# Kernel optimization log

Hardware: AMD Instinct MI355X
Metric: run time of the kernel (lower is better)

The kernel has to match this reference:

```python
import jax, jax.numpy as jnp
import numpy as np

B, IN, E, NCLS = 1024, 784, 256, 10
BRAIN, ADIM, NJUMPS = 4, 3, 4
N = BRAIN ** ADIM  # 64 blocks
TAU = 1.0
_GKEY = jax.random.key(42)  # fixed key -> deterministic gumbel noise


def _gumbel_softmax_hard(key, logits):
    u = jax.random.uniform(key, logits.shape, minval=1e-6, maxval=1.0 - 1e-6)
    g = -jnp.log(-jnp.log(u))
    y = jax.nn.softmax((logits + g) / TAU, axis=-1)
    hard = jax.nn.one_hot(jnp.argmax(y, axis=-1), logits.shape[-1], dtype=y.dtype)
    return jax.lax.stop_gradient(hard - y) + y  # straight-through


def _next_address(state, key, at0_W1, at0_b1, at0_W2, at0_b2):
    # always uses block 0's address_transform (as in the original forward)
    h = jax.nn.relu(state @ at0_W1 + at0_b1)
    logits = (h @ at0_W2 + at0_b2).reshape(state.shape[0], ADIM, BRAIN)
    return _gumbel_softmax_hard(key, logits)  # (B, ADIM, BRAIN) one-hot


def _all_blocks(state, st_W1, st_b1, st_W2, st_b2):
    # state: (B,E); st_W*: (N,E,E) stored (in,out). Two batched GEMMs over all N blocks.
    h = jax.nn.relu(jnp.einsum('be,neh->bnh', state, st_W1) + st_b1[None])
    h = jax.nn.relu(jnp.einsum('bnh,nhg->bng', h, st_W2) + st_b2[None])
    norm = jnp.linalg.norm(state, axis=1, keepdims=True)  # (B,1), norm of INPUT state
    return h / (norm[:, :, None] + 1e-6)  # (B,N,E)


def _flatten_onehot(oh):
    # (B, ADIM, BRAIN) -> (B, BRAIN**ADIM) via iterated outer product
    b = oh.shape[0]
    fw = oh[:, 0, :]
    for d in range(1, oh.shape[1]):
        fw = (fw[:, :, None] * oh[:, d, None, :]).reshape(b, -1)
    return fw


def _forward(x, W_emb, b_emb, st_W1, st_b1, st_W2, st_b2,
             at0_W1, at0_b1, at0_W2, at0_b2, out_W1, out_b1, out_W2, out_b2):
    bsz = x.shape[0]
    state = x.reshape(bsz, -1) @ W_emb + b_emb
    initial_state = state
    current_address = _next_address(state, jax.random.fold_in(_GKEY, 0),
                                    at0_W1, at0_b1, at0_W2, at0_b2)
    exited = jnp.zeros((bsz,), dtype=bool)
    exit_states = jnp.zeros_like(state)
    exit_addresses = jnp.zeros_like(current_address)
    for i in range(NJUMPS):  # fixed small jump count; early-break replaced by masking (same math)
        active = ~exited
        bw = _flatten_onehot(current_address)                      # (B,N)
        allout = _all_blocks(state, st_W1, st_b1, st_W2, st_b2)    # (B,N,E)
        new_state = jnp.einsum('bn,bne->be', bw, allout)
        new_address = _next_address(new_state, jax.random.fold_in(_GKEY, i + 1),
                                    at0_W1, at0_b1, at0_W2, at0_b2)
        idx = jnp.argmax(new_address, axis=2)
        is_origin = jnp.all(idx == 0, axis=1) & active
        exit_states = jnp.where(is_origin[:, None], new_state, exit_states)
        exit_addresses = jnp.where(is_origin[:, None, None], new_address, exit_addresses)
        exited = exited | is_origin
        state = jnp.where(active[:, None], new_state, state)
        current_address = jnp.where(active[:, None, None], new_address, current_address)
    final_address = jnp.where(exited[:, None, None], exit_addresses, current_address)
    bw = _flatten_onehot(final_address)
    # original code computes block_out twice and keeps the one using `state` (bug-faithful)
    allout = _all_blocks(state, st_W1, st_b1, st_W2, st_b2)
    final_output = jnp.einsum('bn,bne->be', bw, allout) + initial_state
    h = jax.nn.relu(final_output @ out_W1 + out_b1)
    return h @ out_W2 + out_b2  # (B, NCLS)


def setup_inputs() -> dict:
    key = jax.random.key(0)
    ks = jax.random.split(key, 16)
    s = 0.02
    return {
        'x': jax.random.normal(ks[0], (B, IN), jnp.float32),
        'W_emb': jax.random.normal(ks[1], (IN, E), jnp.float32) * s,
        'b_emb': jnp.zeros((E,), jnp.float32),
        'st_W1': jax.random.normal(ks[2], (N, E, E), jnp.float32) * s,
        'st_b1': jnp.zeros((N, E), jnp.float32),
        'st_W2': jax.random.normal(ks[3], (N, E, E), jnp.float32) * s,
        'st_b2': jnp.zeros((N, E), jnp.float32),
        'at0_W1': jax.random.normal(ks[4], (E, E), jnp.float32) * s,
        'at0_b1': jnp.zeros((E,), jnp.float32),
        'at0_W2': jax.random.normal(ks[5], (E, ADIM * BRAIN), jnp.float32) * s,
        'at0_b2': jnp.zeros((ADIM * BRAIN,), jnp.float32),
        'out_W1': jax.random.normal(ks[6], (E, E), jnp.float32) * s,
        'out_b1': jnp.zeros((E,), jnp.float32),
        'out_W2': jax.random.normal(ks[7], (E, NCLS), jnp.float32) * s,
        'out_b2': jnp.zeros((NCLS,), jnp.float32),
    }


def reference(x, W_emb, b_emb, st_W1, st_b1, st_W2, st_b2,
              at0_W1, at0_b1, at0_W2, at0_b2, out_W1, out_b1, out_W2, out_b2):
    return _forward(x, W_emb, b_emb, st_W1, st_b1, st_W2, st_b2,
                    at0_W1, at0_b1, at0_W2, at0_b2, out_W1, out_b1, out_W2, out_b2)
```

## Files before the change

kernel.cpp:

```cpp
#include <hip/hip_runtime.h>
#include <stdint.h>


#define BATCH 1024
#define EDIM  256
#define INDIM 784
#define CH    4
#define GRID_B 304

__host__ __device__ inline uint32_t rotl32(uint32_t x, uint32_t d) {
  return (x << d) | (x >> (32u - d));
}
__host__ __device__ inline void threefry2x32(uint32_t k0, uint32_t k1,
                                             uint32_t x0, uint32_t x1,
                                             uint32_t* o0, uint32_t* o1) {
  uint32_t ks2 = k0 ^ k1 ^ 0x1BD11BDAu;
  x0 += k0; x1 += k1;
#define TF_R(a) { x0 += x1; x1 = rotl32(x1, a); x1 ^= x0; }
  TF_R(13) TF_R(15) TF_R(26) TF_R(6)   x0 += k1;  x1 += ks2 + 1u;
  TF_R(17) TF_R(29) TF_R(16) TF_R(24)  x0 += ks2; x1 += k0  + 2u;
  TF_R(13) TF_R(15) TF_R(26) TF_R(6)   x0 += k0;  x1 += k1  + 3u;
  TF_R(17) TF_R(29) TF_R(16) TF_R(24)  x0 += k1;  x1 += ks2 + 4u;
  TF_R(13) TF_R(15) TF_R(26) TF_R(6)   x0 += ks2; x1 += k0  + 5u;
#undef TF_R
  *o0 = x0; *o1 = x1;
}
__device__ inline uint32_t jax_bits12288(uint32_t k0, uint32_t k1, uint32_t L) {
  uint32_t o0, o1;
  if (L < 6144u) { threefry2x32(k0, k1, L, L + 6144u, &o0, &o1); return o0; }
  else           { threefry2x32(k0, k1, L - 6144u, L, &o0, &o1); return o1; }
}
__device__ inline float jax_uniform(uint32_t bits) {
  const float minv = 1e-6f;
  const float maxv = (float)(1.0 - 1e-06);
  const float span = maxv - minv;
  uint32_t fb = (bits >> 9) | 0x3f800000u;
  float f = __uint_as_float(fb) - 1.0f;
  float u = __fadd_rn(__fmul_rn(f, span), minv);
  return fmaxf(minv, u);
}
__device__ inline float gumbel_val(int s, int b, int c) {
  uint32_t fk0, fk1;
  threefry2x32(0u, 42u, 0u, (uint32_t)s, &fk0, &fk1);
  const uint32_t L = (uint32_t)(b * 12 + c);
  const float u = jax_uniform(jax_bits12288(fk0, fk1, L));
  return -logf(-logf(u));
}
__device__ inline int addr_argmax(const float* v) {
  int i0 = 0, i1 = 0, i2 = 0;
  { float b = v[0];
    for (int c = 1; c < 4; c++) { float x = v[c];     if (x > b) { b = x; i0 = c; } } }
  { float b = v[4];
    for (int c = 1; c < 4; c++) { float x = v[4 + c]; if (x > b) { b = x; i1 = c; } } }
  { float b = v[8];
    for (int c = 1; c < 4; c++) { float x = v[8 + c]; if (x > b) { b = x; i2 = c; } } }
  return i0 * 16 + i1 * 4 + i2;
}

#define LDW16(dst, Wc, kkq)                                                     \
  { _Pragma("unroll")                                                           \
    for (int _q = 0; _q < 4; _q++) {                                            \
      _Pragma("unroll")                                                         \
      for (int _cc = 0; _cc < 4; _cc++)                                         \
        dst[_q * 4 + _cc] = (Wc)[(size_t)((kkq) + _q) * EDIM + _cc * 64];       \
    } }

#define FMA16(acc, wv, XSarr, SROW, kabs)                                       \
  { const float4 _r0 = *(const float4*)&(XSarr)[0 * (SROW) + (kabs)];           \
    const float4 _r1 = *(const float4*)&(XSarr)[1 * (SROW) + (kabs)];           \
    const float4 _r2 = *(const float4*)&(XSarr)[2 * (SROW) + (kabs)];           \
    const float4 _r3 = *(const float4*)&(XSarr)[3 * (SROW) + (kabs)];           \
    _Pragma("unroll")                                                           \
    for (int _cc = 0; _cc < 4; _cc++) {                                         \
      acc[0][_cc] = fmaf(_r0.x, wv[0 + _cc], acc[0][_cc]);                      \
      acc[0][_cc] = fmaf(_r0.y, wv[4 + _cc], acc[0][_cc]);                      \
      acc[0][_cc] = fmaf(_r0.z, wv[8 + _cc], acc[0][_cc]);                      \
      acc[0][_cc] = fmaf(_r0.w, wv[12 + _cc], acc[0][_cc]);                     \
      acc[1][_cc] = fmaf(_r1.x, wv[0 + _cc], acc[1][_cc]);                      \
      acc[1][_cc] = fmaf(_r1.y, wv[4 + _cc], acc[1][_cc]);                      \
      acc[1][_cc] = fmaf(_r1.z, wv[8 + _cc], acc[1][_cc]);                      \
      acc[1][_cc] = fmaf(_r1.w, wv[12 + _cc], acc[1][_cc]);                     \
      acc[2][_cc] = fmaf(_r2.x, wv[0 + _cc], acc[2][_cc]);                      \
      acc[2][_cc] = fmaf(_r2.y, wv[4 + _cc], acc[2][_cc]);                      \
      acc[2][_cc] = fmaf(_r2.z, wv[8 + _cc], acc[2][_cc]);                      \
      acc[2][_cc] = fmaf(_r2.w, wv[12 + _cc], acc[2][_cc]);                     \
      acc[3][_cc] = fmaf(_r3.x, wv[0 + _cc], acc[3][_cc]);                      \
      acc[3][_cc] = fmaf(_r3.y, wv[4 + _cc], acc[3][_cc]);                      \
      acc[3][_cc] = fmaf(_r3.z, wv[8 + _cc], acc[3][_cc]);                      \
      acc[3][_cc] = fmaf(_r3.w, wv[12 + _cc], acc[3][_cc]);                     \
    } }

#define GEMM_TILE(Wbase, XSarr, SROW, kb, KS, acc)                              \
  { const float* _Wc = (Wbase) + (size_t)(kb) * EDIM + jc;                      \
    float _wvA[16], _wvB[16];                                                   \
    LDW16(_wvA, _Wc, 0)                                                         \
    _Pragma("unroll 1")                                                         \
    for (int _kk = 0; _kk < (KS); _kk += 8) {                                   \
      LDW16(_wvB, _Wc, _kk + 4)                                                 \
      FMA16(acc, _wvA, XSarr, SROW, (kb) + _kk)                                 \
      if (_kk + 8 < (KS)) LDW16(_wvA, _Wc, _kk + 8)                             \
      FMA16(acc, _wvB, XSarr, SROW, (kb) + _kk + 4)                             \
    } }

#define FMA16H(acc, wv, Harr, kabs)                                             \
  { _Pragma("unroll")                                                           \
    for (int _q = 0; _q < 4; _q++) {                                            \
      const float4 _h = *(const float4*)&(Harr)[((kabs) + _q) * 4];             \
      _Pragma("unroll")                                                         \
      for (int _cc = 0; _cc < 4; _cc++) {                                       \
        acc[0][_cc] = fmaf(_h.x, wv[_q * 4 + _cc], acc[0][_cc]);                \
        acc[1][_cc] = fmaf(_h.y, wv[_q * 4 + _cc], acc[1][_cc]);                \
        acc[2][_cc] = fmaf(_h.z, wv[_q * 4 + _cc], acc[2][_cc]);                \
        acc[3][_cc] = fmaf(_h.w, wv[_q * 4 + _cc], acc[3][_cc]);                \
      } } }

#define GEMM_TILE_H(Wbase, Harr, kb, KS, acc)                                   \
  { const float* _Wc = (Wbase) + (size_t)(kb) * EDIM + jc;                      \
    float _wvA[16], _wvB[16];                                                   \
    LDW16(_wvA, _Wc, 0)                                                         \
    _Pragma("unroll 1")                                                         \
    for (int _kk = 0; _kk < (KS); _kk += 8) {                                   \
      LDW16(_wvB, _Wc, _kk + 4)                                                 \
      FMA16H(acc, _wvA, Harr, (kb) + _kk)                                       \
      if (_kk + 8 < (KS)) LDW16(_wvA, _Wc, _kk + 8)                             \
      FMA16H(acc, _wvB, Harr, (kb) + _kk + 4)                                   \
    } }

#define P_STORE(P, kg, jc, acc)                                                 \
  { _Pragma("unroll")                                                           \
    for (int _cc = 0; _cc < 4; _cc++) {                                         \
      const int _col = (jc) + _cc * 64;                                         \
      *(float4*)&(P)[(((kg) * 256) + _col) * 4] =                               \
        make_float4(acc[0][_cc], acc[1][_cc], acc[2][_cc], acc[3][_cc]);        \
    } }

#define P_REDUCE8(P, col, bias, dst4)                                           \
  { float4 _ps = *(const float4*)&(P)[(col) * 4];                               \
    _Pragma("unroll")                                                           \
    for (int _pw = 1; _pw < 8; _pw++) {                                         \
      const float4 _pp = *(const float4*)&(P)[((_pw * 256) + (col)) * 4];       \
      _ps.x += _pp.x; _ps.y += _pp.y; _ps.z += _pp.z; _ps.w += _pp.w;           \
    }                                                                           \
    _ps.x += (bias); _ps.y += (bias); _ps.z += (bias); _ps.w += (bias);         \
    dst4 = _ps; }

#define ADDR_TAIL(P, H, P2a, vals, ab1, aW2, ab2, astep, b0)                    \
  { if (t < 256) {                                                              \
      float4 s; P_REDUCE8(P, t, (ab1)[t], s);                                   \
      *(float4*)&(H)[t * 4] = make_float4(fmaxf(s.x, 0.f), fmaxf(s.y, 0.f),     \
                                          fmaxf(s.z, 0.f), fmaxf(s.w, 0.f));    \
    }                                                                           \
    __syncthreads();                                                            \
    { const int c = t & 15, ksl = t >> 4;                                       \
      float a2[4] = {0.f, 0.f, 0.f, 0.f};                                       \
      if (c < 12) {                                                             \
        const int k0 = ksl * 8;                                                 \
        _Pragma("unroll")                                                       \
        for (int k = k0; k < k0 + 8; k++) {                                     \
          const float4 h = *(const float4*)&(H)[k * 4];                         \
          const float w = (aW2)[k * 12 + c];                                    \
          a2[0] = fmaf(h.x, w, a2[0]); a2[1] = fmaf(h.y, w, a2[1]);             \
          a2[2] = fmaf(h.z, w, a2[2]); a2[3] = fmaf(h.w, w, a2[3]);             \
        }                                                                       \
      }                                                                         \
      *(float4*)&(P2a)[(ksl * 16 + c) * 4] = make_float4(a2[0], a2[1], a2[2], a2[3]); \
    }                                                                           \
    __syncthreads();                                                            \
    if (t < 48) {                                                               \
      const int i = t / 12, c = t % 12;                                         \
      float s = 0.f;                                                            \
      _Pragma("unroll")                                                         \
      for (int w = 0; w < 32; w++) s += (P2a)[(w * 16 + c) * 4 + i];            \
      (vals)[i * 12 + c] = s + (ab2)[c] + gumbel_val((astep), (b0) + i, c);     \
    }                                                                           \
    __syncthreads();                                                            \
  }

__global__ __launch_bounds__(512, 2) void k_embed_a0(
    const float* __restrict__ x, const float* __restrict__ Wemb,
    const float* __restrict__ bemb,
    const float* __restrict__ aW1, const float* __restrict__ ab1,
    const float* __restrict__ aW2, const float* __restrict__ ab2,
    float* __restrict__ state, float* __restrict__ initial,
    int* __restrict__ nn_all) {
  __shared__ __align__(16) float XS[4 * INDIM];
  __shared__ __align__(16) float P[8 * 256 * 4];
  __shared__ __align__(16) float SS[4 * EDIM];
  __shared__ __align__(16) float H[EDIM * 4];
  __shared__ __align__(16) float P2a[32 * 16 * 4];
  __shared__ float vals[4 * 12];
  const int t = threadIdx.x, b0 = blockIdx.x * 4;
  const int jc = t & 63, kg = t >> 6;

  { const float4* src = (const float4*)(x + (size_t)b0 * INDIM);
    for (int p = t; p < INDIM; p += 512) ((float4*)XS)[p] = src[p];
  }
  __syncthreads();

  {
    const int kb = (kg < 2) ? kg * 104 : 208 + (kg - 2) * 96;
    float acc[4][4] = {};
    if (kg < 2) { GEMM_TILE(Wemb, XS, INDIM, kb, 104, acc); }
    else        { GEMM_TILE(Wemb, XS, INDIM, kb, 96, acc); }
    P_STORE(P, kg, jc, acc);
  }
  __syncthreads();
  if (t < 256) {
    float4 s; P_REDUCE8(P, t, bemb[t], s);
    SS[0 * EDIM + t] = s.x; SS[1 * EDIM + t] = s.y;
    SS[2 * EDIM + t] = s.z; SS[3 * EDIM + t] = s.w;
    state[(size_t)(b0 + 0) * EDIM + t] = s.x; initial[(size_t)(b0 + 0) * EDIM + t] = s.x;
    state[(size_t)(b0 + 1) * EDIM + t] = s.y; initial[(size_t)(b0 + 1) * EDIM + t] = s.y;
    state[(size_t)(b0 + 2) * EDIM + t] = s.z; initial[(size_t)(b0 + 2) * EDIM + t] = s.z;
    state[(size_t)(b0 + 3) * EDIM + t] = s.w; initial[(size_t)(b0 + 3) * EDIM + t] = s.w;
  }
  __syncthreads();

  {
    const int kb = kg * 32;
    float acc[4][4] = {};
    GEMM_TILE(aW1, SS, EDIM, kb, 32, acc);
    P_STORE(P, kg, jc, acc);
  }
  __syncthreads();
  ADDR_TAIL(P, H, P2a, vals, ab1, aW2, ab2, 0, b0);
  if (t < 4) nn_all[b0 + t] = addr_argmax(&vals[t * 12]);
}

__global__ __launch_bounds__(512, 2) void k_addr(
    const float* __restrict__ state,
    const float* __restrict__ aW1, const float* __restrict__ ab1,
    const float* __restrict__ aW2, const float* __restrict__ ab2,
    const int* __restrict__ nn_prev, int* __restrict__ nn_out, int step) {
  __shared__ __align__(16) float XS[4 * EDIM];
  __shared__ __align__(16) float P[8 * 256 * 4];
  __shared__ __align__(16) float H[EDIM * 4];
  __shared__ __align__(16) float P2a[32 * 16 * 4];
  __shared__ float vals[4 * 12];
  const int t = threadIdx.x, b0 = blockIdx.x * 4;
  const int jc = t & 63, kg = t >> 6;

  if (t < 256) ((float4*)XS)[t] = ((const float4*)(state + (size_t)b0 * EDIM))[t];
  __syncthreads();

  { const int kb = kg * 32;
    float acc[4][4] = {};
    GEMM_TILE(aW1, XS, EDIM, kb, 32, acc);
    P_STORE(P, kg, jc, acc);
  }
  __syncthreads();
  ADDR_TAIL(P, H, P2a, vals, ab1, aW2, ab2, step, b0);
  if (t < 4) {
    const int b = b0 + t;
    int nxt;
    if (nn_prev[b] < 0) nxt = -1;
    else {
      const int nn = addr_argmax(&vals[t * 12]);
      nxt = (step < 4 && nn == 0) ? -1 : nn;
    }
    nn_out[b] = nxt;
  }
}

#define B_ROUTE(nnval_expr)                                                     \
  if (t < 64) hist[t] = 0;                                                      \
  if (t < 4) rowsl[t] = 0;                                                      \
  __syncthreads();                                                              \
  int myv[2]; bool fl[2];                                                       \
  _Pragma("unroll")                                                             \
  for (int p = 0; p < 2; p++) {                                                 \
    const int rr = p * 512 + t;                                                 \
    myv[p] = (nnval_expr);                                                      \
    if (myv[p] >= 0) atomicAdd(&hist[myv[p]], 1);                               \
  }                                                                             \
  __syncthreads();                                                              \
  if (t < 64) {                                                                 \
    const int cnt = hist[t];                                                    \
    const int nch = (cnt + CH - 1) / CH;                                        \
    int icnt = cnt, inch = nch;                                                 \
    _Pragma("unroll")                                                           \
    for (int d = 1; d < 64; d <<= 1) {                                          \
      int t1 = __shfl_up(icnt, d), t2 = __shfl_up(inch, d);                     \
      if (t >= d) { icnt += t1; inch += t2; }                                   \
    }                                                                           \
    const int ench = inch - nch;                                                \
    if (t == 63) meta[3] = inch;                                                \
    if (c >= ench && c < ench + nch) {                                          \
      meta[0] = t; meta[1] = c - ench;                                          \
      meta[2] = min(CH, cnt - (c - ench) * CH);                                 \
    }                                                                           \
  }                                                                             \
  __syncthreads();                                                              \
  if (c >= meta[3]) return;                                                     \
  const int n = meta[0], local = meta[1], m = meta[2];                          \
  {                                                                             \
    const int wid = t >> 6, lane = t & 63;                                      \
    unsigned long long bals[2];                                                 \
    _Pragma("unroll")                                                           \
    for (int p = 0; p < 2; p++) {                                               \
      fl[p] = (myv[p] == n);                                                    \
      bals[p] = __ballot(fl[p]);                                                \
      if (lane == 0) wcnt2[p * 8 + wid] = __popcll(bals[p]);                    \
    }                                                                           \
    __syncthreads();                                                            \
    if (t == 0) { int s = 0;                                                    \
      for (int e = 0; e < 16; e++) { wbase2[e] = s; s += wcnt2[e]; } }          \
    __syncthreads();                                                            \
    const int r0 = local * CH;                                                  \
    _Pragma("unroll")                                                           \
    for (int p = 0; p < 2; p++) {                                               \
      if (fl[p]) {                                                              \
        const int rank = wbase2[p * 8 + wid] +                                  \
          __popcll(bals[p] & ((1ull << lane) - 1ull));                          \
        if (rank >= r0 && rank < r0 + CH) rowsl[rank - r0] = p * 512 + t;       \
      }                                                                         \
    }                                                                           \
    __syncthreads();                                                            \
  }

__global__ __launch_bounds__(512, 2) void k_blocks(
    float* __restrict__ state,
    const float* __restrict__ W1, const float* __restrict__ b1,
    const float* __restrict__ W2, const float* __restrict__ b2,
    const int* __restrict__ nnj) {
  __shared__ __align__(16) float XS[4 * EDIM];
  __shared__ __align__(16) float P[8 * 256 * 4];
  __shared__ __align__(16) float H[EDIM * 4];
  __shared__ int hist[64], meta[4], rowsl[4];
  __shared__ int wcnt2[16], wbase2[16];
  __shared__ float denom[4];
  const int t = threadIdx.x;
  const int c = ((blockIdx.x & 7) * 38) + (blockIdx.x >> 3);
  const int jc = t & 63, kg = t >> 6;

  B_ROUTE(nnj[rr])

  if (t < 256) {
    const int i = t >> 6, q = t & 63;
    const int row = rowsl[min(i, m - 1)] & 1023;
    const float4 v = *(const float4*)(state + (size_t)row * EDIM + q * 4);
    ((float4*)XS)[t] = v;
    float sq = v.x * v.x + v.y * v.y + v.z * v.z + v.w * v.w;
#pragma unroll
    for (int d = 32; d >= 1; d >>= 1) sq += __shfl_xor(sq, d);
    if (q == 0) denom[i] = sqrtf(sq) + 1e-6f;
  }
  __syncthreads();

  const float* W1n = W1 + (size_t)n * EDIM * EDIM;
  const float* W2n = W2 + (size_t)n * EDIM * EDIM;
  const int kb = kg * 32;
  { float acc[4][4] = {};
    GEMM_TILE(W1n, XS, EDIM, kb, 32, acc);
    P_STORE(P, kg, jc, acc);
  }
  __syncthreads();
  if (t < 256) {
    float4 s; P_REDUCE8(P, t, b1[(size_t)n * EDIM + t], s);
    *(float4*)&H[t * 4] = make_float4(fmaxf(s.x, 0.f), fmaxf(s.y, 0.f),
                                      fmaxf(s.z, 0.f), fmaxf(s.w, 0.f));
  }
  __syncthreads();
  { float acc[4][4] = {};
    GEMM_TILE_H(W2n, H, kb, 32, acc);
    P_STORE(P, kg, jc, acc);
  }
  __syncthreads();
  if (t < 256) {
    float4 s; P_REDUCE8(P, t, b2[(size_t)n * EDIM + t], s);
    float sv[4] = { s.x, s.y, s.z, s.w };
#pragma unroll
    for (int i = 0; i < 4; i++) {
      if (i < m) {
        const int row = rowsl[i] & 1023;
        state[(size_t)row * EDIM + t] = fmaxf(sv[i], 0.f) / denom[i];
      }
    }
  }
}

__global__ __launch_bounds__(512, 2) void k_block_final(
    const float* __restrict__ state,
    const float* __restrict__ W1, const float* __restrict__ b1,
    const float* __restrict__ W2, const float* __restrict__ b2,
    const float* __restrict__ initial,
    const float* __restrict__ oW1, const float* __restrict__ ob1,
    const float* __restrict__ oW2, const float* __restrict__ ob2,
    const int* __restrict__ nn4, float* __restrict__ out) {
  __shared__ __align__(16) float XS[4 * EDIM];
  __shared__ __align__(16) float P[8 * 256 * 4];
  __shared__ __align__(16) float H[EDIM * 4];
  __shared__ __align__(16) float P2h[32 * 16 * 4];
  __shared__ int hist[64], meta[4], rowsl[4];
  __shared__ int wcnt2[16], wbase2[16];
  __shared__ float denom[4];
  const int t = threadIdx.x;
  const int c = ((blockIdx.x & 7) * 38) + (blockIdx.x >> 3);
  const int jc = t & 63, kg = t >> 6;

  B_ROUTE(max(nn4[rr], 0))

  if (t < 256) {
    const int i = t >> 6, q = t & 63;
    const int row = rowsl[min(i, m - 1)] & 1023;
    const float4 v = *(const float4*)(state + (size_t)row * EDIM + q * 4);
    ((float4*)XS)[t] = v;
    float sq = v.x * v.x + v.y * v.y + v.z * v.z + v.w * v.w;
#pragma unroll
    for (int d = 32; d >= 1; d >>= 1) sq += __shfl_xor(sq, d);
    if (q == 0) denom[i] = sqrtf(sq) + 1e-6f;
  }
  __syncthreads();

  const float* W1n = W1 + (size_t)n * EDIM * EDIM;
  const float* W2n = W2 + (size_t)n * EDIM * EDIM;
  const int kb = kg * 32;
  { float acc[4][4] = {};
    GEMM_TILE(W1n, XS, EDIM, kb, 32, acc);
    P_STORE(P, kg, jc, acc);
  }
  __syncthreads();
  if (t < 256) {
    float4 s; P_REDUCE8(P, t, b1[(size_t)n * EDIM + t], s);
    *(float4*)&H[t * 4] = make_float4(fmaxf(s.x, 0.f), fmaxf(s.y, 0.f),
                                      fmaxf(s.z, 0.f), fmaxf(s.w, 0.f));
  }
  __syncthreads();
  { float acc[4][4] = {};
    GEMM_TILE_H(W2n, H, kb, 32, acc);
    P_STORE(P, kg, jc, acc);
  }
  __syncthreads();
  if (t < 256) {
    float4 s; P_REDUCE8(P, t, b2[(size_t)n * EDIM + t], s);
    float sv[4] = { s.x, s.y, s.z, s.w };
#pragma unroll
    for (int i = 0; i < 4; i++) {
      const int row = rowsl[i] & 1023;
      float v = fmaxf(sv[i], 0.f) / denom[i];
      v += initial[(size_t)row * EDIM + t];
      XS[i * EDIM + t] = v;
    }
  }
  __syncthreads();

  { float acc[4][4] = {};
    GEMM_TILE(oW1, XS, EDIM, kb, 32, acc);
    P_STORE(P, kg, jc, acc);
  }
  __syncthreads();
  if (t < 256) {
    float4 s; P_REDUCE8(P, t, ob1[t], s);
    *(float4*)&H[t * 4] = make_float4(fmaxf(s.x, 0.f), fmaxf(s.y, 0.f),
                                      fmaxf(s.z, 0.f), fmaxf(s.w, 0.f));
  }
  __syncthreads();
  {
    const int cc = t & 15, ksl = t >> 4;
    float a2[4] = {0.f, 0.f, 0.f, 0.f};
    if (cc < 10) {
      const int k0 = ksl * 8;
#pragma unroll
      for (int k = k0; k < k0 + 8; k++) {
        const float4 h = *(const float4*)&H[k * 4];
        const float w = oW2[k * 10 + cc];
        a2[0] = fmaf(h.x, w, a2[0]); a2[1] = fmaf(h.y, w, a2[1]);
        a2[2] = fmaf(h.z, w, a2[2]); a2[3] = fmaf(h.w, w, a2[3]);
      }
    }
    *(float4*)&P2h[(ksl * 16 + cc) * 4] = make_float4(a2[0], a2[1], a2[2], a2[3]);
  }
  __syncthreads();
  if (t < 40) {
    const int i = t / 10, cc = t % 10;
    if (i < m) {
      float s = 0.f;
#pragma unroll
      for (int w = 0; w < 32; w++) s += P2h[(w * 16 + cc) * 4 + i];
      const int row = rowsl[i] & 1023;
      out[(size_t)row * 10 + cc] = s + ob2[cc];
    }
  }
}

extern "C" void kernel_launch(void* const* d_in, const int* in_sizes, int n_in,
                              void* d_out, int out_size, void* d_ws, size_t ws_size,
                              hipStream_t stream) {
  const float* x    = (const float*)d_in[0];
  const float* Wemb = (const float*)d_in[1];
  const float* bemb = (const float*)d_in[2];
  const float* stW1 = (const float*)d_in[3];
  const float* stb1 = (const float*)d_in[4];
  const float* stW2 = (const float*)d_in[5];
  const float* stb2 = (const float*)d_in[6];
  const float* aW1  = (const float*)d_in[7];
  const float* ab1  = (const float*)d_in[8];
  const float* aW2  = (const float*)d_in[9];
  const float* ab2  = (const float*)d_in[10];
  const float* oW1  = (const float*)d_in[11];
  const float* ob1  = (const float*)d_in[12];
  const float* oW2  = (const float*)d_in[13];
  const float* ob2  = (const float*)d_in[14];
  float* out = (float*)d_out;

  char* ws = (char*)d_ws;
  auto alloc = [&](size_t bytes) { char* p = ws; ws += (bytes + 255) & ~(size_t)255; return p; };
  float* state   = (float*)alloc((size_t)BATCH * EDIM * 4);
  float* initial = (float*)alloc((size_t)BATCH * EDIM * 4);
  int*   nn_all  = (int*)alloc(5 * BATCH * 4);

  k_embed_a0<<<BATCH / 4, 512, 0, stream>>>(x, Wemb, bemb, aW1, ab1, aW2, ab2,
                                            state, initial, nn_all);
  for (int j = 0; j < 4; j++) {
    k_blocks<<<GRID_B, 512, 0, stream>>>(state, stW1, stb1, stW2, stb2,
                                         nn_all + j * BATCH);
    k_addr<<<BATCH / 4, 512, 0, stream>>>(state, aW1, ab1, aW2, ab2,
                                          nn_all + j * BATCH,
                                          nn_all + (j + 1) * BATCH, j + 1);
  }
  k_block_final<<<GRID_B, 512, 0, stream>>>(state, stW1, stb1, stW2, stb2,
                                            initial, oW1, ob1, oW2, ob2,
                                            nn_all + 4 * BATCH, out);
}
```

Baseline: 227.3 us.

## Fuse address-transform step into the routed block kernel

Removes the separate k_addr launch after each jump. Each routed block kernel now computes the next address for the rows it just processed, using the new state still held in shared memory. When a row's address picks block 0 before the last step, all its future routing slots are set to -1. This saves four kernel launches and a global reload of state, but adds the address GEMM and its tail to every block-kernel workgroup, which lengthens those workgroups.

```diff
diff --git a/kernel.cpp b/kernel.cpp
--- a/kernel.cpp
+++ b/kernel.cpp
@@ -144,7 +144,7 @@
     _ps.x += (bias); _ps.y += (bias); _ps.z += (bias); _ps.w += (bias);         \
     dst4 = _ps; }
 
-#define ADDR_TAIL(P, H, P2a, vals, ab1, aW2, ab2, astep, b0)                    \
+#define ADDR_TAIL(P, H, P2a, vals, ab1, aW2, ab2, astep, ROWEXPR)               \
   { if (t < 256) {                                                              \
       float4 s; P_REDUCE8(P, t, (ab1)[t], s);                                   \
       *(float4*)&(H)[t * 4] = make_float4(fmaxf(s.x, 0.f), fmaxf(s.y, 0.f),     \
@@ -171,7 +171,7 @@
       float s = 0.f;                                                            \
       _Pragma("unroll")                                                         \
       for (int w = 0; w < 32; w++) s += (P2a)[(w * 16 + c) * 4 + i];            \
-      (vals)[i * 12 + c] = s + (ab2)[c] + gumbel_val((astep), (b0) + i, c);     \
+      (vals)[i * 12 + c] = s + (ab2)[c] + gumbel_val((astep), (ROWEXPR), c);    \
     }                                                                           \
     __syncthreads();                                                            \
   }
@@ -223,43 +223,8 @@
     P_STORE(P, kg, jc, acc);
   }
   __syncthreads();
-  ADDR_TAIL(P, H, P2a, vals, ab1, aW2, ab2, 0, b0);
+  ADDR_TAIL(P, H, P2a, vals, ab1, aW2, ab2, 0, b0 + i);
   if (t < 4) nn_all[b0 + t] = addr_argmax(&vals[t * 12]);
-}
-
-__global__ __launch_bounds__(512, 2) void k_addr(
-    const float* __restrict__ state,
-    const float* __restrict__ aW1, const float* __restrict__ ab1,
-    const float* __restrict__ aW2, const float* __restrict__ ab2,
-    const int* __restrict__ nn_prev, int* __restrict__ nn_out, int step) {
-  __shared__ __align__(16) float XS[4 * EDIM];
-  __shared__ __align__(16) float P[8 * 256 * 4];
-  __shared__ __align__(16) float H[EDIM * 4];
-  __shared__ __align__(16) float P2a[32 * 16 * 4];
-  __shared__ float vals[4 * 12];
-  const int t = threadIdx.x, b0 = blockIdx.x * 4;
-  const int jc = t & 63, kg = t >> 6;
-
-  if (t < 256) ((float4*)XS)[t] = ((const float4*)(state + (size_t)b0 * EDIM))[t];
-  __syncthreads();
-
-  { const int kb = kg * 32;
-    float acc[4][4] = {};
-    GEMM_TILE(aW1, XS, EDIM, kb, 32, acc);
-    P_STORE(P, kg, jc, acc);
-  }
-  __syncthreads();
-  ADDR_TAIL(P, H, P2a, vals, ab1, aW2, ab2, step, b0);
-  if (t < 4) {
-    const int b = b0 + t;
-    int nxt;
-    if (nn_prev[b] < 0) nxt = -1;
-    else {
-      const int nn = addr_argmax(&vals[t * 12]);
-      nxt = (step < 4 && nn == 0) ? -1 : nn;
-    }
-    nn_out[b] = nxt;
-  }
 }
 
 #define B_ROUTE(nnval_expr)                                                     \
@@ -318,20 +283,25 @@
     __syncthreads();                                                            \
   }
 
-__global__ __launch_bounds__(512, 2) void k_blocks(
+__global__ __launch_bounds__(512, 2) void k_block_mid(
     float* __restrict__ state,
     const float* __restrict__ W1, const float* __restrict__ b1,
     const float* __restrict__ W2, const float* __restrict__ b2,
-    const int* __restrict__ nnj) {
+    const float* __restrict__ aW1, const float* __restrict__ ab1,
+    const float* __restrict__ aW2, const float* __restrict__ ab2,
+    int* __restrict__ nn_all, int rstep) {
   __shared__ __align__(16) float XS[4 * EDIM];
   __shared__ __align__(16) float P[8 * 256 * 4];
   __shared__ __align__(16) float H[EDIM * 4];
+  __shared__ __align__(16) float P2a[32 * 16 * 4];
+  __shared__ float vals[4 * 12];
   __shared__ int hist[64], meta[4], rowsl[4];
   __shared__ int wcnt2[16], wbase2[16];
   __shared__ float denom[4];
   const int t = threadIdx.x;
   const int c = ((blockIdx.x & 7) * 38) + (blockIdx.x >> 3);
   const int jc = t & 63, kg = t >> 6;
+  const int* nnj = nn_all + rstep * BATCH;
 
   B_ROUTE(nnj[rr])
 
@@ -373,9 +343,29 @@
     for (int i = 0; i < 4; i++) {
       if (i < m) {
         const int row = rowsl[i] & 1023;
-        state[(size_t)row * EDIM + t] = fmaxf(sv[i], 0.f) / denom[i];
+        const float v = fmaxf(sv[i], 0.f) / denom[i];
+        state[(size_t)row * EDIM + t] = v;
+        XS[i * EDIM + t] = v;
       }
     }
+  }
+  __syncthreads();
+
+  { float acc[4][4] = {};
+    GEMM_TILE(aW1, XS, EDIM, kb, 32, acc);
+    P_STORE(P, kg, jc, acc);
+  }
+  __syncthreads();
+  ADDR_TAIL(P, H, P2a, vals, ab1, aW2, ab2, rstep + 1, (rowsl[i] & 1023));
+  if (t < m) {
+    const int b = rowsl[t] & 1023;
+    const int nn = addr_argmax(&vals[t * 12]);
+    const int s = rstep + 1;
+    if (s < 4) {
+      if (nn == 0) {
+        for (int q = s; q <= 4; q++) nn_all[q * BATCH + b] = -1;
+      } else nn_all[s * BATCH + b] = nn;
+    } else nn_all[4 * BATCH + b] = nn;
   }
 }
 
@@ -511,13 +501,9 @@
 
   k_embed_a0<<<BATCH / 4, 512, 0, stream>>>(x, Wemb, bemb, aW1, ab1, aW2, ab2,
                                             state, initial, nn_all);
-  for (int j = 0; j < 4; j++) {
-    k_blocks<<<GRID_B, 512, 0, stream>>>(state, stW1, stb1, stW2, stb2,
-                                         nn_all + j * BATCH);
-    k_addr<<<BATCH / 4, 512, 0, stream>>>(state, aW1, ab1, aW2, ab2,
-                                          nn_all + j * BATCH,
-                                          nn_all + (j + 1) * BATCH, j + 1);
-  }
+  for (int j = 0; j < 4; j++)
+    k_block_mid<<<GRID_B, 512, 0, stream>>>(state, stW1, stb1, stW2, stb2,
+                                            aW1, ab1, aW2, ab2, nn_all, j);
   k_block_final<<<GRID_B, 512, 0, stream>>>(state, stW1, stb1, stW2, stb2,
                                             initial, oW1, ob1, oW2, ob2,
                                             nn_all + 4 * BATCH, out);
```

Result: no change. 231.3 us (+1.8%).
